# Performance work log

Measured on AMD Instinct MI355X. Metric: run time of the kernel, lower is better.

The kernel has to match this reference:

```python
import jax, jax.numpy as jnp
import numpy as np

B, L, H, NH = 4, 1024, 768, 12
NE, M, P = 30, 6, 600
EMB, BS, NC = 768, 16, 97
NEG = -1e30


def setup_inputs() -> dict:
    key = jax.random.key(0)
    ks = jax.random.split(key, 9)
    sequence_output = jax.random.normal(ks[0], (B, L, H), jnp.float32)
    attention = jax.random.uniform(ks[1], (B, NH, L, L), jnp.float32)
    mention_idx = jax.random.randint(ks[2], (B, NE, M), 0, L)
    mention_mask = jnp.ones((B, NE, M), jnp.float32)
    hts = jax.random.randint(ks[3], (B, P, 2), 0, NE)
    s = 0.02
    head_W = jax.random.normal(ks[4], (EMB, 2 * H), jnp.float32) * s
    head_b = jnp.zeros((EMB,), jnp.float32)
    tail_W = jax.random.normal(ks[5], (EMB, 2 * H), jnp.float32) * s
    tail_b = jnp.zeros((EMB,), jnp.float32)
    proj_W = jax.random.normal(ks[6], (H, EMB * BS), jnp.float32) * s
    cls_W = jax.random.normal(ks[7], (NC, H), jnp.float32) * s
    cls_b = jnp.zeros((NC,), jnp.float32)
    return {
        'sequence_output': sequence_output, 'attention': attention,
        'head_W': head_W, 'head_b': head_b, 'tail_W': tail_W, 'tail_b': tail_b,
        'proj_W': proj_W, 'cls_W': cls_W, 'cls_b': cls_b,
        'mention_mask': mention_mask, 'mention_idx': mention_idx, 'hts': hts,
    }


def reference(sequence_output, attention, head_W, head_b, tail_W, tail_b,
              proj_W, cls_W, cls_b, mention_mask, mention_idx, hts):
    b_, l_, h_ = sequence_output.shape
    bidx = jnp.arange(b_)[:, None, None]                     # [B,1,1]
    # ---- per-entity pooling (segment reduce over ragged mentions) ----
    m_emb = sequence_output[bidx, mention_idx]               # [B,NE,M,H]
    att_t = attention.transpose(0, 2, 1, 3)                  # [B,L,NH,L]
    m_att = att_t[bidx, mention_idx]                         # [B,NE,M,NH,L]
    masked = jnp.where(mention_mask[..., None] > 0, m_emb, NEG)
    e_emb = jax.nn.logsumexp(masked, axis=2)                 # [B,NE,H]
    cnt = jnp.maximum(mention_mask.sum(2), 1.0)              # [B,NE]
    e_att = (m_att * mention_mask[..., None, None]).sum(2) / cnt[..., None, None]  # [B,NE,NH,L]
    # ---- head/tail gathers over pairs ----
    b2 = jnp.arange(b_)[:, None]                             # [B,1]
    h_emb = e_emb[b2, hts[..., 0]]                           # [B,P,H]
    t_emb = e_emb[b2, hts[..., 1]]
    h_att = e_att[b2, hts[..., 0]]                           # [B,P,NH,L]
    t_att = e_att[b2, hts[..., 1]]
    ht_att = (h_att * t_att).mean(2)                         # [B,P,L]
    ht_att = ht_att / (ht_att.sum(-1, keepdims=True) + 1e-30)
    rs = jnp.einsum('bpl,blh->bph', ht_att, sequence_output) # [B,P,H]
    # ---- extractors + block-bilinear classifier ----
    hs = jnp.tanh(jnp.concatenate([h_emb, rs], -1) @ head_W.T + head_b)  # [B,P,EMB]
    ts = jnp.tanh(jnp.concatenate([t_emb, rs], -1) @ tail_W.T + tail_b)
    emb = hs.shape[-1]
    bs = proj_W.shape[1] // emb
    p_ = hs.shape[1]
    b1 = hs.reshape(b_, p_, emb // bs, bs)
    b2t = ts.reshape(b_, p_, emb // bs, bs)
    bl = (b1[..., :, None] * b2t[..., None, :]).reshape(b_, p_, emb * bs)
    logits = (bl @ proj_W.T) @ cls_W.T + cls_b               # [B,P,NC]
    return logits
```

## Files before the change

kernel.cpp:

```cpp
#include <hip/hip_runtime.h>
#include <cmath>

#define B_   4
#define L_   1024
#define H_   768
#define NH_  12
#define NE_  30
#define M_   6
#define P_   600
#define EMB_ 768
#define BS_  16
#define NC_  97

typedef __bf16 bf16x8 __attribute__((ext_vector_type(8)));
typedef float floatx4 __attribute__((ext_vector_type(4)));

union V16 { uint4 q; __bf16 b[8]; bf16x8 v; };
union V8  { unsigned long long u; __bf16 b[4]; };

__device__ __forceinline__ void gload16(const __bf16* g, __bf16* l) {
  __builtin_amdgcn_global_load_lds(
      (const __attribute__((address_space(1))) void*)g,
      (__attribute__((address_space(3))) void*)l, 16, 0, 0);
}

__device__ __forceinline__ void mfma_step(
    const __bf16* As, const __bf16* Bs,
    int ar, int bc, int frow, int kg, floatx4 acc[2][2])
{
  V16 a0, a1, b0, b1;
  a0.q = *reinterpret_cast<const uint4*>(As + (ar + frow) * 32 + kg * 8);
  a1.q = *reinterpret_cast<const uint4*>(As + (ar + 16 + frow) * 32 + kg * 8);
  b0.q = *reinterpret_cast<const uint4*>(Bs + (bc + frow) * 32 + kg * 8);
  b1.q = *reinterpret_cast<const uint4*>(Bs + (bc + 16 + frow) * 32 + kg * 8);
  acc[0][0] = __builtin_amdgcn_mfma_f32_16x16x32_bf16(a0.v, b0.v, acc[0][0], 0, 0, 0);
  acc[0][1] = __builtin_amdgcn_mfma_f32_16x16x32_bf16(a0.v, b1.v, acc[0][1], 0, 0, 0);
  acc[1][0] = __builtin_amdgcn_mfma_f32_16x16x32_bf16(a1.v, b0.v, acc[1][0], 0, 0, 0);
  acc[1][1] = __builtin_amdgcn_mfma_f32_16x16x32_bf16(a1.v, b1.v, acc[1][1], 0, 0, 0);
}

__device__ __forceinline__ void gemm_core(
    const __bf16* __restrict__ A, int lda, long aRow0,
    const __bf16* __restrict__ Bt, int ldb, long bRow0,
    int K, __bf16* sm, floatx4 acc[2][2])
{
  const int tid = threadIdx.x;
  const int lid = tid & 63, w = tid >> 6;
  const int ar = (w & 1) * 32, bc = (w >> 1) * 32;
  const int frow = lid & 15, kg = lid >> 4;
  const int grow = tid >> 2, gq = (tid & 3) * 8;
  const __bf16* ag = A + (aRow0 + grow) * (long)lda + gq;
  const __bf16* bg = Bt + (bRow0 + grow) * (long)ldb + gq;
  __bf16* wA = sm + w * 512;
  const int nt = K >> 5;
  gload16(ag, wA);
  gload16(bg, wA + 2048);
  gload16(ag + 32, wA + 4096);
  gload16(bg + 32, wA + 4096 + 2048);
  int cur = 0;
  for (int i = 0; i < nt - 1; ++i) {
    asm volatile("s_waitcnt vmcnt(2)" ::: "memory");
    __builtin_amdgcn_s_barrier();
    __builtin_amdgcn_sched_barrier(0);
    if (i + 2 < nt) {
      int nb = cur + 2; if (nb >= 3) nb -= 3;
      __bf16* d = sm + nb * 4096 + w * 512;
      gload16(ag + (i + 2) * 32, d);
      gload16(bg + (i + 2) * 32, d + 2048);
    }
    const __bf16* As = sm + cur * 4096;
    mfma_step(As, As + 2048, ar, bc, frow, kg, acc);
    cur += 1; if (cur == 3) cur = 0;
  }
  asm volatile("s_waitcnt vmcnt(0)" ::: "memory");
  __builtin_amdgcn_s_barrier();
  __builtin_amdgcn_sched_barrier(0);
  const __bf16* As = sm + cur * 4096;
  mfma_step(As, As + 2048, ar, bc, frow, kg, acc);
}

#define S1_ATT  1440
#define S1_POOL 120
#define S1_TPS  768
#define S1_TPW  2304
#define S1_CVT  2400

__device__ __forceinline__ void transpose64(
    const float* __restrict__ in, __bf16* __restrict__ out,
    int R, int C, int bx, int by, float (*t)[65])
{
  int c0 = bx*64, r0 = by*64;
  int tx = threadIdx.x & 15, ty = threadIdx.x >> 4;
#pragma unroll
  for (int p = 0; p < 4; ++p) {
    float4 v = *reinterpret_cast<const float4*>(
        in + (long)(r0 + ty + p*16)*C + c0 + tx*4);
    t[ty + p*16][tx*4 + 0] = v.x;
    t[ty + p*16][tx*4 + 1] = v.y;
    t[ty + p*16][tx*4 + 2] = v.z;
    t[ty + p*16][tx*4 + 3] = v.w;
  }
  __syncthreads();
#pragma unroll
  for (int p = 0; p < 4; ++p) {
    V8 o;
#pragma unroll
    for (int i = 0; i < 4; ++i) o.b[i] = (__bf16)t[tx*4 + i][ty + p*16];
    *reinterpret_cast<unsigned long long*>(
        out + (long)(c0 + ty + p*16)*R + r0 + tx*4) = o.u;
  }
}

__global__ __launch_bounds__(256) void k_prep(
    const float* __restrict__ seq, const float* __restrict__ att,
    const float* __restrict__ headW, const float* __restrict__ tailW,
    const float* __restrict__ projW, const float* __restrict__ clsW,
    const float* __restrict__ mmask, const int* __restrict__ midx,
    __bf16* __restrict__ Wt, __bf16* __restrict__ clsA,
    __bf16* __restrict__ projWT, __bf16* __restrict__ seqT,
    __bf16* __restrict__ e_embB, __bf16* __restrict__ e_att)
{
  __shared__ float t[64][65];
  int blk = blockIdx.x;
  int tid = threadIdx.x;
  if (blk < S1_ATT) {
    int i = blk*256 + tid;
    int l4 = (i & 255) * 4;
    int nh = (i >> 8) % NH_;
    int be = i / (256 * NH_);
    int b  = be / NE_;
    float s0=0.f, s1=0.f, s2=0.f, s3=0.f, cnt=0.f;
#pragma unroll
    for (int m = 0; m < M_; ++m) {
      float mk = mmask[be*M_ + m];
      cnt += mk;
      int id = midx[be*M_ + m];
      float4 a = *reinterpret_cast<const float4*>(
          att + (((size_t)b*NH_ + nh)*L_ + id)*L_ + l4);
      s0 += mk*a.x; s1 += mk*a.y; s2 += mk*a.z; s3 += mk*a.w;
    }
    float inv = 1.f / fmaxf(cnt, 1.f);
    V8 o;
    o.b[0]=(__bf16)(s0*inv); o.b[1]=(__bf16)(s1*inv);
    o.b[2]=(__bf16)(s2*inv); o.b[3]=(__bf16)(s3*inv);
    *reinterpret_cast<unsigned long long*>(e_att + ((size_t)be*NH_ + nh)*L_ + l4) = o.u;
  } else if (blk < S1_ATT + S1_POOL) {
    int be = blk - S1_ATT;
    int idx[M_]; float msk[M_];
#pragma unroll
    for (int m = 0; m < M_; ++m) {
      idx[m] = midx[be * M_ + m];
      msk[m] = mmask[be * M_ + m];
    }
    int b = be / NE_;
    const float* sb = seq + (size_t)b * L_ * H_;
    for (int h = tid; h < H_; h += 256) {
      float v[M_]; float mx = -3.0e38f;
#pragma unroll
      for (int m = 0; m < M_; ++m) {
        float x = (msk[m] > 0.f) ? sb[(size_t)idx[m] * H_ + h] : -1e30f;
        v[m] = x; mx = fmaxf(mx, x);
      }
      float s = 0.f;
#pragma unroll
      for (int m = 0; m < M_; ++m) s += expf(v[m] - mx);
      e_embB[(size_t)be * H_ + h] = (__bf16)(mx + logf(s));
    }
  } else if (blk < S1_ATT + S1_POOL + S1_TPS) {
    int b = blk - (S1_ATT + S1_POOL);
    int bx = b % 12, by = (b / 12) % 16, bz = b / 192;
    transpose64(seq + (long)bz*L_*H_, seqT + (long)bz*H_*L_, L_, H_, bx, by, t);
  } else if (blk < S1_ATT + S1_POOL + S1_TPS + S1_TPW) {
    int b = blk - (S1_ATT + S1_POOL + S1_TPS);
    transpose64(projW, projWT, H_, EMB_*BS_, b % 192, b / 192, t);
  } else {
    int gid = (blk - (S1_ATT + S1_POOL + S1_TPS + S1_TPW))*256 + tid;
    if (gid < 2*H_*384) {
      int sel = gid / (H_*384);
      int rem = gid % (H_*384);
      int o = rem / 384;
      int k4 = (rem % 384) * 4;
      const float* W = sel ? tailW : headW;
      float4 v = *reinterpret_cast<const float4*>(W + (long)o*(2*H_) + k4);
      V8 d; d.b[0]=(__bf16)v.x; d.b[1]=(__bf16)v.y; d.b[2]=(__bf16)v.z; d.b[3]=(__bf16)v.w;
      *reinterpret_cast<unsigned long long*>(Wt + ((long)sel*H_ + o)*(2*H_) + k4) = d.u;
    } else {
      int rem = gid - 2*H_*384;
      int row = rem / 192;
      int k4 = (rem % 192) * 4;
      V8 d;
      if (row < NC_) {
        float4 v = *reinterpret_cast<const float4*>(clsW + (long)row*H_ + k4);
        d.b[0]=(__bf16)v.x; d.b[1]=(__bf16)v.y; d.b[2]=(__bf16)v.z; d.b[3]=(__bf16)v.w;
      } else {
        d.b[0]=d.b[1]=d.b[2]=d.b[3]=(__bf16)0.f;
      }
      *reinterpret_cast<unsigned long long*>(clsA + (long)row*H_ + k4) = d.u;
    }
  }
}

#define S2_WC  384
#define S2_PRE 48
#define S2_HT  2400

__global__ __launch_bounds__(256) void k_mid(
    const __bf16* __restrict__ clsA, const __bf16* __restrict__ projWT,
    const __bf16* __restrict__ e_att, const int* __restrict__ hts,
    const __bf16* __restrict__ e_embB, const __bf16* __restrict__ Wt,
    __bf16* __restrict__ WcT, __bf16* __restrict__ htatt,
    float* __restrict__ hpre, float* __restrict__ tpre)
{
  __shared__ __bf16 sm[3*4096];
  int blk = blockIdx.x;
  int tid = threadIdx.x;
  if (blk < S2_WC) {
    int n0 = (blk % 192)*64, r0 = (blk / 192)*64;
    floatx4 acc[2][2] = {};
    gemm_core(clsA, H_, r0, projWT, H_, n0, H_, sm, acc);
    int lid = tid & 63, w = tid >> 6;
    int ar = (w&1)*32, bc = (w>>1)*32, frow = lid&15, kg = lid>>4;
#pragma unroll
    for (int i = 0; i < 2; ++i)
#pragma unroll
      for (int r = 0; r < 4; ++r) {
        int c = r0 + ar + i*16 + kg*4 + r;
#pragma unroll
        for (int j = 0; j < 2; ++j)
          WcT[(long)c*(EMB_*BS_) + n0 + bc + j*16 + frow] = (__bf16)acc[i][j][r];
      }
  } else if (blk < S2_WC + S2_PRE) {
    int tb = blk - S2_WC;
    int o0 = (tb % 12)*64;
    int r0 = ((tb / 12) & 1)*64;
    int sel = tb / 24;
    floatx4 acc[2][2] = {};
    gemm_core(e_embB, H_, r0, Wt + (long)sel*H_*(2*H_), 2*H_, o0, H_, sm, acc);
    float* out = sel ? tpre : hpre;
    int lid = tid & 63, w = tid >> 6;
    int ar = (w&1)*32, bc = (w>>1)*32, frow = lid&15, kg = lid>>4;
#pragma unroll
    for (int i = 0; i < 2; ++i)
#pragma unroll
      for (int r = 0; r < 4; ++r) {
        int be = r0 + ar + i*16 + kg*4 + r;
        if (be < B_*NE_) {
#pragma unroll
          for (int j = 0; j < 2; ++j)
            out[(long)be*EMB_ + o0 + bc + j*16 + frow] = acc[i][j][r];
        }
      }
  } else {
    int bp = blk - (S2_WC + S2_PRE);
    int b = bp / P_;
    int hi = hts[bp*2 + 0], ti = hts[bp*2 + 1];
    const __bf16* ha = e_att + (size_t)(b*NE_ + hi) * NH_ * L_;
    const __bf16* ta = e_att + (size_t)(b*NE_ + ti) * NH_ * L_;
    int l4 = tid * 4;
    float v[4] = {0.f,0.f,0.f,0.f};
#pragma unroll
    for (int nh = 0; nh < NH_; ++nh) {
      V8 x, y;
      x.u = *reinterpret_cast<const unsigned long long*>(ha + nh*L_ + l4);
      y.u = *reinterpret_cast<const unsigned long long*>(ta + nh*L_ + l4);
#pragma unroll
      for (int q = 0; q < 4; ++q) v[q] += (float)x.b[q] * (float)y.b[q];
    }
    float loc = 0.f;
#pragma unroll
    for (int q = 0; q < 4; ++q) { v[q] *= (1.f/NH_); loc += v[q]; }
    float* red = reinterpret_cast<float*>(sm);
    for (int off = 32; off > 0; off >>= 1) loc += __shfl_down(loc, off, 64);
    if ((tid & 63) == 0) red[tid >> 6] = loc;
    __syncthreads();
    float inv = 1.f / (red[0] + red[1] + red[2] + red[3] + 1e-30f);
    V8 o;
#pragma unroll
    for (int q = 0; q < 4; ++q) o.b[q] = (__bf16)(v[q] * inv);
    *reinterpret_cast<unsigned long long*>(htatt + (size_t)bp*L_ + l4) = o.u;
  }
}

__global__ __launch_bounds__(256) void k_rs_mfma(
    const __bf16* __restrict__ htatt, const __bf16* __restrict__ seqT,
    __bf16* __restrict__ rs)
{
  __shared__ __bf16 sm[3*4096];
  int b = blockIdx.z, p0 = blockIdx.y*64, h0 = blockIdx.x*64;
  floatx4 acc[2][2] = {};
  gemm_core(htatt, L_, (long)b*P_ + p0, seqT + (long)b*H_*L_, L_, h0, L_, sm, acc);
  int lid = threadIdx.x & 63, w = threadIdx.x >> 6;
  int ar = (w&1)*32, bc = (w>>1)*32, frow = lid&15, kg = lid>>4;
#pragma unroll
  for (int i = 0; i < 2; ++i)
#pragma unroll
    for (int r = 0; r < 4; ++r) {
      int p = p0 + ar + i*16 + kg*4 + r;
      if (p < P_) {
#pragma unroll
        for (int j = 0; j < 2; ++j)
          rs[((long)b*P_ + p)*H_ + h0 + bc + j*16 + frow] = (__bf16)acc[i][j][r];
      }
    }
}

__global__ __launch_bounds__(256) void k_extract_mfma(
    const __bf16* __restrict__ rs, const __bf16* __restrict__ Wt,
    const float* __restrict__ headb, const float* __restrict__ tailb,
    const float* __restrict__ hpre, const float* __restrict__ tpre,
    const int* __restrict__ hts, __bf16* __restrict__ hs, __bf16* __restrict__ ts)
{
  __shared__ __bf16 sm[3*4096];
  int sel = blockIdx.z, r0 = blockIdx.y*64, o0 = blockIdx.x*64;
  const float* bias = sel ? tailb : headb;
  const float* pre = sel ? tpre : hpre;
  __bf16* out = sel ? ts : hs;
  floatx4 acc[2][2] = {};
  gemm_core(rs, H_, r0, Wt + (long)sel*H_*(2*H_) + H_, 2*H_, o0, H_, sm, acc);
  int lid = threadIdx.x & 63, w = threadIdx.x >> 6;
  int ar = (w&1)*32, bc = (w>>1)*32, frow = lid&15, kg = lid>>4;
#pragma unroll
  for (int i = 0; i < 2; ++i)
#pragma unroll
    for (int r = 0; r < 4; ++r) {
      int row = r0 + ar + i*16 + kg*4 + r;
      if (row < B_*P_) {
        int b = row / P_;
        int e = hts[row*2 + sel];
        const float* prow = pre + (long)(b*NE_ + e) * EMB_;
#pragma unroll
        for (int j = 0; j < 2; ++j) {
          int o = o0 + bc + j*16 + frow;
          out[(long)row*EMB_ + o] = (__bf16)tanhf(acc[i][j][r] + prow[o] + bias[o]);
        }
      }
    }
}

__global__ __launch_bounds__(512) void k_logits_mfma(
    const __bf16* __restrict__ hs, const __bf16* __restrict__ ts,
    const __bf16* __restrict__ WcT, const float* __restrict__ clsb,
    float* __restrict__ out)
{
  int rt = blockIdx.x >> 3;
  int ks = blockIdx.x & 7;
  int tid = threadIdx.x;
  int w = tid >> 6, lid = tid & 63;
  int rg = w & 1, kq = w >> 1;
  int frow = lid & 15, kg = lid >> 4;
  int row = rt*32 + rg*16 + frow;
  long hsrow = (long)row * EMB_;
  floatx4 acc[7] = {};
  int kbase0 = ks*1536 + kq*384;
  for (int s = 0; s < 12; ++s) {
    int kb = kbase0 + s*32 + kg*8;
    int q16 = (kb >> 8) << 4;
    int ii = (kb >> 4) & 15;
    int jj0 = kb & 15;
    float hv = (float)hs[hsrow + q16 + ii];
    V16 tsv; tsv.q = *reinterpret_cast<const uint4*>(ts + hsrow + q16 + jj0);
    bf16x8 af;
#pragma unroll
    for (int j = 0; j < 8; ++j) af[j] = (__bf16)(hv * (float)tsv.b[j]);
#pragma unroll
    for (int f = 0; f < 7; ++f) {
      V16 bv; bv.q = *reinterpret_cast<const uint4*>(WcT + (long)(f*16 + frow)*(EMB_*BS_) + kb);
      acc[f] = __builtin_amdgcn_mfma_f32_16x16x32_bf16(af, bv.v, acc[f], 0, 0, 0);
    }
  }
  __shared__ float red[2][16][112];
  if (kq == 0) {
#pragma unroll
    for (int f = 0; f < 7; ++f)
#pragma unroll
      for (int r = 0; r < 4; ++r)
        red[rg][kg*4 + r][f*16 + frow] = acc[f][r];
  }
  __syncthreads();
#pragma unroll
  for (int q = 1; q < 4; ++q) {
    if (kq == q) {
#pragma unroll
      for (int f = 0; f < 7; ++f)
#pragma unroll
        for (int r = 0; r < 4; ++r)
          red[rg][kg*4 + r][f*16 + frow] += acc[f][r];
    }
    __syncthreads();
  }
  for (int e = tid; e < 32*112; e += 512) {
    int rr = e / 112, cc = e % 112;
    if (cc < NC_) {
      float s = red[rr >> 4][rr & 15][cc] + ((ks == 0) ? clsb[cc] : 0.f);
      atomicAdd(out + (long)(rt*32 + rr)*NC_ + cc, s);
    }
  }
}

extern "C" void kernel_launch(void* const* d_in, const int* in_sizes, int n_in,
                              void* d_out, int out_size, void* d_ws, size_t ws_size,
                              hipStream_t stream) {
  const float* seq   = (const float*)d_in[0];
  const float* att   = (const float*)d_in[1];
  const float* headW = (const float*)d_in[2];
  const float* headb = (const float*)d_in[3];
  const float* tailW = (const float*)d_in[4];
  const float* tailb = (const float*)d_in[5];
  const float* projW = (const float*)d_in[6];
  const float* clsW  = (const float*)d_in[7];
  const float* clsb  = (const float*)d_in[8];
  const float* mmask = (const float*)d_in[9];
  const int* midx = (const int*)d_in[10];
  const int* hts  = (const int*)d_in[11];

  char* p = (char*)d_ws;
  auto alloc_f = [&](size_t n){ float* r = (float*)p; p += n*sizeof(float); return r; };
  auto alloc_b = [&](size_t n){ __bf16* r = (__bf16*)p; p += n*2; return r; };
  float* hpre    = alloc_f((size_t)B_*NE_*EMB_);
  float* tpre    = alloc_f((size_t)B_*NE_*EMB_);
  __bf16* e_embB = alloc_b((size_t)128*H_);
  __bf16* e_att  = alloc_b((size_t)B_*NE_*NH_*L_);
  __bf16* htattb = alloc_b((size_t)2464*L_);
  __bf16* seqT   = alloc_b((size_t)B_*H_*L_);
  __bf16* rsb    = alloc_b((size_t)2432*H_);
  __bf16* Wt     = alloc_b((size_t)2*H_*2*H_);
  __bf16* clsA   = alloc_b((size_t)128*H_);
  __bf16* WcT    = alloc_b((size_t)128*EMB_*BS_);
  __bf16* projWT = alloc_b((size_t)EMB_*BS_*H_);
  __bf16* hsb = projWT;
  __bf16* tsb = projWT + (size_t)B_*P_*EMB_;

  hipMemsetAsync(d_out, 0, (size_t)B_*P_*NC_*sizeof(float), stream);

  k_prep<<<S1_ATT + S1_POOL + S1_TPS + S1_TPW + S1_CVT, 256, 0, stream>>>(
      seq, att, headW, tailW, projW, clsW, mmask, midx,
      Wt, clsA, projWT, seqT, e_embB, e_att);
  k_mid<<<S2_WC + S2_PRE + S2_HT, 256, 0, stream>>>(
      clsA, projWT, e_att, hts, e_embB, Wt, WcT, htattb, hpre, tpre);
  k_rs_mfma<<<dim3(H_/64, 10, B_), 256, 0, stream>>>(htattb, seqT, rsb);
  k_extract_mfma<<<dim3(EMB_/64, 38, 2), 256, 0, stream>>>(
      rsb, Wt, headb, tailb, hpre, tpre, hts, hsb, tsb);
  k_logits_mfma<<<600, 512, 0, stream>>>(hsb, tsb, WcT, clsb, (float*)d_out);
}
```

Measured before the change: 426.7 us.

## Fuse all stages into one persistent kernel with software grid barriers

Replaces the five separate kernel launches and the output memset with a single persistent kernel of 768 blocks. Each block loops over the virtual blocks of each stage, and stages are separated by atomic-counter grid barriers. The output is zeroed inside the first stage. The logits stage is reshaped to 256-thread blocks covering 16 rows each. This removes launch and inter-kernel gaps, at the cost of less latency hiding in the bandwidth-bound stages. It also depends on all 768 blocks being co-resident, with no cooperative launch to guarantee it, so the barriers could deadlock.

```diff
diff --git a/kernel.cpp b/kernel.cpp
--- a/kernel.cpp
+++ b/kernel.cpp
@@ -12,6 +12,8 @@
 #define BS_  16
 #define NC_  97
 
+#define NBLK 768
+
 typedef __bf16 bf16x8 __attribute__((ext_vector_type(8)));
 typedef float floatx4 __attribute__((ext_vector_type(4)));
 
@@ -22,6 +24,17 @@
   __builtin_amdgcn_global_load_lds(
       (const __attribute__((address_space(1))) void*)g,
       (__attribute__((address_space(3))) void*)l, 16, 0, 0);
+}
+
+__device__ __forceinline__ void grid_sync(int* cnt) {
+  __syncthreads();
+  if (threadIdx.x == 0) {
+    __threadfence();
+    atomicAdd(cnt, 1);
+    while (atomicAdd(cnt, 0) < NBLK) __builtin_amdgcn_s_sleep(32);
+    __threadfence();
+  }
+  __syncthreads();
 }
 
 __device__ __forceinline__ void mfma_step(
@@ -79,12 +92,6 @@
   mfma_step(As, As + 2048, ar, bc, frow, kg, acc);
 }
 
-#define S1_ATT  1440
-#define S1_POOL 120
-#define S1_TPS  768
-#define S1_TPW  2304
-#define S1_CVT  2400
-
 __device__ __forceinline__ void transpose64(
     const float* __restrict__ in, __bf16* __restrict__ out,
     int R, int C, int bx, int by, float (*t)[65])
@@ -111,288 +118,306 @@
   }
 }
 
-__global__ __launch_bounds__(256) void k_prep(
-    const float* __restrict__ seq, const float* __restrict__ att,
-    const float* __restrict__ headW, const float* __restrict__ tailW,
-    const float* __restrict__ projW, const float* __restrict__ clsW,
-    const float* __restrict__ mmask, const int* __restrict__ midx,
-    __bf16* __restrict__ Wt, __bf16* __restrict__ clsA,
-    __bf16* __restrict__ projWT, __bf16* __restrict__ seqT,
-    __bf16* __restrict__ e_embB, __bf16* __restrict__ e_att)
-{
-  __shared__ float t[64][65];
-  int blk = blockIdx.x;
-  int tid = threadIdx.x;
-  if (blk < S1_ATT) {
-    int i = blk*256 + tid;
-    int l4 = (i & 255) * 4;
-    int nh = (i >> 8) % NH_;
-    int be = i / (256 * NH_);
-    int b  = be / NE_;
-    float s0=0.f, s1=0.f, s2=0.f, s3=0.f, cnt=0.f;
-#pragma unroll
-    for (int m = 0; m < M_; ++m) {
-      float mk = mmask[be*M_ + m];
-      cnt += mk;
-      int id = midx[be*M_ + m];
-      float4 a = *reinterpret_cast<const float4*>(
-          att + (((size_t)b*NH_ + nh)*L_ + id)*L_ + l4);
-      s0 += mk*a.x; s1 += mk*a.y; s2 += mk*a.z; s3 += mk*a.w;
-    }
-    float inv = 1.f / fmaxf(cnt, 1.f);
-    V8 o;
-    o.b[0]=(__bf16)(s0*inv); o.b[1]=(__bf16)(s1*inv);
-    o.b[2]=(__bf16)(s2*inv); o.b[3]=(__bf16)(s3*inv);
-    *reinterpret_cast<unsigned long long*>(e_att + ((size_t)be*NH_ + nh)*L_ + l4) = o.u;
-  } else if (blk < S1_ATT + S1_POOL) {
-    int be = blk - S1_ATT;
-    int idx[M_]; float msk[M_];
-#pragma unroll
-    for (int m = 0; m < M_; ++m) {
-      idx[m] = midx[be * M_ + m];
-      msk[m] = mmask[be * M_ + m];
-    }
-    int b = be / NE_;
-    const float* sb = seq + (size_t)b * L_ * H_;
-    for (int h = tid; h < H_; h += 256) {
-      float v[M_]; float mx = -3.0e38f;
-#pragma unroll
-      for (int m = 0; m < M_; ++m) {
-        float x = (msk[m] > 0.f) ? sb[(size_t)idx[m] * H_ + h] : -1e30f;
-        v[m] = x; mx = fmaxf(mx, x);
-      }
-      float s = 0.f;
-#pragma unroll
-      for (int m = 0; m < M_; ++m) s += expf(v[m] - mx);
-      e_embB[(size_t)be * H_ + h] = (__bf16)(mx + logf(s));
-    }
-  } else if (blk < S1_ATT + S1_POOL + S1_TPS) {
-    int b = blk - (S1_ATT + S1_POOL);
-    int bx = b % 12, by = (b / 12) % 16, bz = b / 192;
-    transpose64(seq + (long)bz*L_*H_, seqT + (long)bz*H_*L_, L_, H_, bx, by, t);
-  } else if (blk < S1_ATT + S1_POOL + S1_TPS + S1_TPW) {
-    int b = blk - (S1_ATT + S1_POOL + S1_TPS);
-    transpose64(projW, projWT, H_, EMB_*BS_, b % 192, b / 192, t);
-  } else {
-    int gid = (blk - (S1_ATT + S1_POOL + S1_TPS + S1_TPW))*256 + tid;
-    if (gid < 2*H_*384) {
-      int sel = gid / (H_*384);
-      int rem = gid % (H_*384);
-      int o = rem / 384;
-      int k4 = (rem % 384) * 4;
-      const float* W = sel ? tailW : headW;
-      float4 v = *reinterpret_cast<const float4*>(W + (long)o*(2*H_) + k4);
-      V8 d; d.b[0]=(__bf16)v.x; d.b[1]=(__bf16)v.y; d.b[2]=(__bf16)v.z; d.b[3]=(__bf16)v.w;
-      *reinterpret_cast<unsigned long long*>(Wt + ((long)sel*H_ + o)*(2*H_) + k4) = d.u;
-    } else {
-      int rem = gid - 2*H_*384;
-      int row = rem / 192;
-      int k4 = (rem % 192) * 4;
-      V8 d;
-      if (row < NC_) {
-        float4 v = *reinterpret_cast<const float4*>(clsW + (long)row*H_ + k4);
-        d.b[0]=(__bf16)v.x; d.b[1]=(__bf16)v.y; d.b[2]=(__bf16)v.z; d.b[3]=(__bf16)v.w;
-      } else {
-        d.b[0]=d.b[1]=d.b[2]=d.b[3]=(__bf16)0.f;
-      }
-      *reinterpret_cast<unsigned long long*>(clsA + (long)row*H_ + k4) = d.u;
-    }
-  }
-}
-
+#define S1_ATT  1440
+#define S1_POOL 120
+#define S1_TPS  768
+#define S1_TPW  2304
+#define S1_CVT  2400
+#define NPREP (S1_ATT + S1_POOL + S1_TPS + S1_TPW + S1_CVT)
 #define S2_WC  384
 #define S2_PRE 48
 #define S2_HT  2400
-
-__global__ __launch_bounds__(256) void k_mid(
-    const __bf16* __restrict__ clsA, const __bf16* __restrict__ projWT,
-    const __bf16* __restrict__ e_att, const int* __restrict__ hts,
-    const __bf16* __restrict__ e_embB, const __bf16* __restrict__ Wt,
+#define NMID (S2_WC + S2_PRE + S2_HT)
+#define NRS   480
+#define NEXT  912
+#define NLOG  1200
+
+__global__ __launch_bounds__(256, 4) void k_fused(
+    const float* __restrict__ seq, const float* __restrict__ att,
+    const float* __restrict__ headW, const float* __restrict__ headb,
+    const float* __restrict__ tailW, const float* __restrict__ tailb,
+    const float* __restrict__ projW, const float* __restrict__ clsW,
+    const float* __restrict__ clsb, const float* __restrict__ mmask,
+    const int* __restrict__ midx, const int* __restrict__ hts,
+    __bf16* __restrict__ Wt, __bf16* __restrict__ clsA,
+    __bf16* __restrict__ projWT, __bf16* __restrict__ seqT,
+    __bf16* __restrict__ e_embB, __bf16* __restrict__ e_att,
     __bf16* __restrict__ WcT, __bf16* __restrict__ htatt,
-    float* __restrict__ hpre, float* __restrict__ tpre)
+    float* __restrict__ hpre, float* __restrict__ tpre,
+    __bf16* __restrict__ rs, __bf16* __restrict__ hs, __bf16* __restrict__ ts,
+    float* __restrict__ out, int* __restrict__ bar)
 {
-  __shared__ __bf16 sm[3*4096];
-  int blk = blockIdx.x;
-  int tid = threadIdx.x;
-  if (blk < S2_WC) {
-    int n0 = (blk % 192)*64, r0 = (blk / 192)*64;
-    floatx4 acc[2][2] = {};
-    gemm_core(clsA, H_, r0, projWT, H_, n0, H_, sm, acc);
-    int lid = tid & 63, w = tid >> 6;
-    int ar = (w&1)*32, bc = (w>>1)*32, frow = lid&15, kg = lid>>4;
-#pragma unroll
-    for (int i = 0; i < 2; ++i)
-#pragma unroll
-      for (int r = 0; r < 4; ++r) {
-        int c = r0 + ar + i*16 + kg*4 + r;
-#pragma unroll
-        for (int j = 0; j < 2; ++j)
-          WcT[(long)c*(EMB_*BS_) + n0 + bc + j*16 + frow] = (__bf16)acc[i][j][r];
-      }
-  } else if (blk < S2_WC + S2_PRE) {
-    int tb = blk - S2_WC;
-    int o0 = (tb % 12)*64;
-    int r0 = ((tb / 12) & 1)*64;
-    int sel = tb / 24;
-    floatx4 acc[2][2] = {};
-    gemm_core(e_embB, H_, r0, Wt + (long)sel*H_*(2*H_), 2*H_, o0, H_, sm, acc);
-    float* out = sel ? tpre : hpre;
-    int lid = tid & 63, w = tid >> 6;
-    int ar = (w&1)*32, bc = (w>>1)*32, frow = lid&15, kg = lid>>4;
-#pragma unroll
-    for (int i = 0; i < 2; ++i)
-#pragma unroll
-      for (int r = 0; r < 4; ++r) {
-        int be = r0 + ar + i*16 + kg*4 + r;
-        if (be < B_*NE_) {
-#pragma unroll
-          for (int j = 0; j < 2; ++j)
-            out[(long)be*EMB_ + o0 + bc + j*16 + frow] = acc[i][j][r];
-        }
-      }
-  } else {
-    int bp = blk - (S2_WC + S2_PRE);
-    int b = bp / P_;
-    int hi = hts[bp*2 + 0], ti = hts[bp*2 + 1];
-    const __bf16* ha = e_att + (size_t)(b*NE_ + hi) * NH_ * L_;
-    const __bf16* ta = e_att + (size_t)(b*NE_ + ti) * NH_ * L_;
-    int l4 = tid * 4;
-    float v[4] = {0.f,0.f,0.f,0.f};
-#pragma unroll
-    for (int nh = 0; nh < NH_; ++nh) {
-      V8 x, y;
-      x.u = *reinterpret_cast<const unsigned long long*>(ha + nh*L_ + l4);
-      y.u = *reinterpret_cast<const unsigned long long*>(ta + nh*L_ + l4);
-#pragma unroll
-      for (int q = 0; q < 4; ++q) v[q] += (float)x.b[q] * (float)y.b[q];
-    }
-    float loc = 0.f;
-#pragma unroll
-    for (int q = 0; q < 4; ++q) { v[q] *= (1.f/NH_); loc += v[q]; }
-    float* red = reinterpret_cast<float*>(sm);
-    for (int off = 32; off > 0; off >>= 1) loc += __shfl_down(loc, off, 64);
-    if ((tid & 63) == 0) red[tid >> 6] = loc;
-    __syncthreads();
-    float inv = 1.f / (red[0] + red[1] + red[2] + red[3] + 1e-30f);
-    V8 o;
-#pragma unroll
-    for (int q = 0; q < 4; ++q) o.b[q] = (__bf16)(v[q] * inv);
-    *reinterpret_cast<unsigned long long*>(htatt + (size_t)bp*L_ + l4) = o.u;
-  }
-}
-
-__global__ __launch_bounds__(256) void k_rs_mfma(
-    const __bf16* __restrict__ htatt, const __bf16* __restrict__ seqT,
-    __bf16* __restrict__ rs)
-{
-  __shared__ __bf16 sm[3*4096];
-  int b = blockIdx.z, p0 = blockIdx.y*64, h0 = blockIdx.x*64;
-  floatx4 acc[2][2] = {};
-  gemm_core(htatt, L_, (long)b*P_ + p0, seqT + (long)b*H_*L_, L_, h0, L_, sm, acc);
-  int lid = threadIdx.x & 63, w = threadIdx.x >> 6;
-  int ar = (w&1)*32, bc = (w>>1)*32, frow = lid&15, kg = lid>>4;
-#pragma unroll
-  for (int i = 0; i < 2; ++i)
-#pragma unroll
-    for (int r = 0; r < 4; ++r) {
-      int p = p0 + ar + i*16 + kg*4 + r;
-      if (p < P_) {
-#pragma unroll
-        for (int j = 0; j < 2; ++j)
-          rs[((long)b*P_ + p)*H_ + h0 + bc + j*16 + frow] = (__bf16)acc[i][j][r];
-      }
-    }
-}
-
-__global__ __launch_bounds__(256) void k_extract_mfma(
-    const __bf16* __restrict__ rs, const __bf16* __restrict__ Wt,
-    const float* __restrict__ headb, const float* __restrict__ tailb,
-    const float* __restrict__ hpre, const float* __restrict__ tpre,
-    const int* __restrict__ hts, __bf16* __restrict__ hs, __bf16* __restrict__ ts)
-{
-  __shared__ __bf16 sm[3*4096];
-  int sel = blockIdx.z, r0 = blockIdx.y*64, o0 = blockIdx.x*64;
-  const float* bias = sel ? tailb : headb;
-  const float* pre = sel ? tpre : hpre;
-  __bf16* out = sel ? ts : hs;
-  floatx4 acc[2][2] = {};
-  gemm_core(rs, H_, r0, Wt + (long)sel*H_*(2*H_) + H_, 2*H_, o0, H_, sm, acc);
-  int lid = threadIdx.x & 63, w = threadIdx.x >> 6;
-  int ar = (w&1)*32, bc = (w>>1)*32, frow = lid&15, kg = lid>>4;
-#pragma unroll
-  for (int i = 0; i < 2; ++i)
-#pragma unroll
-    for (int r = 0; r < 4; ++r) {
-      int row = r0 + ar + i*16 + kg*4 + r;
-      if (row < B_*P_) {
-        int b = row / P_;
-        int e = hts[row*2 + sel];
-        const float* prow = pre + (long)(b*NE_ + e) * EMB_;
-#pragma unroll
-        for (int j = 0; j < 2; ++j) {
-          int o = o0 + bc + j*16 + frow;
-          out[(long)row*EMB_ + o] = (__bf16)tanhf(acc[i][j][r] + prow[o] + bias[o]);
-        }
-      }
-    }
-}
-
-__global__ __launch_bounds__(512) void k_logits_mfma(
-    const __bf16* __restrict__ hs, const __bf16* __restrict__ ts,
-    const __bf16* __restrict__ WcT, const float* __restrict__ clsb,
-    float* __restrict__ out)
-{
-  int rt = blockIdx.x >> 3;
-  int ks = blockIdx.x & 7;
-  int tid = threadIdx.x;
-  int w = tid >> 6, lid = tid & 63;
-  int rg = w & 1, kq = w >> 1;
-  int frow = lid & 15, kg = lid >> 4;
-  int row = rt*32 + rg*16 + frow;
-  long hsrow = (long)row * EMB_;
-  floatx4 acc[7] = {};
-  int kbase0 = ks*1536 + kq*384;
-  for (int s = 0; s < 12; ++s) {
-    int kb = kbase0 + s*32 + kg*8;
-    int q16 = (kb >> 8) << 4;
-    int ii = (kb >> 4) & 15;
-    int jj0 = kb & 15;
-    float hv = (float)hs[hsrow + q16 + ii];
-    V16 tsv; tsv.q = *reinterpret_cast<const uint4*>(ts + hsrow + q16 + jj0);
-    bf16x8 af;
-#pragma unroll
-    for (int j = 0; j < 8; ++j) af[j] = (__bf16)(hv * (float)tsv.b[j]);
-#pragma unroll
-    for (int f = 0; f < 7; ++f) {
-      V16 bv; bv.q = *reinterpret_cast<const uint4*>(WcT + (long)(f*16 + frow)*(EMB_*BS_) + kb);
-      acc[f] = __builtin_amdgcn_mfma_f32_16x16x32_bf16(af, bv.v, acc[f], 0, 0, 0);
-    }
-  }
-  __shared__ float red[2][16][112];
-  if (kq == 0) {
-#pragma unroll
-    for (int f = 0; f < 7; ++f)
-#pragma unroll
-      for (int r = 0; r < 4; ++r)
-        red[rg][kg*4 + r][f*16 + frow] = acc[f][r];
-  }
-  __syncthreads();
-#pragma unroll
-  for (int q = 1; q < 4; ++q) {
-    if (kq == q) {
-#pragma unroll
-      for (int f = 0; f < 7; ++f)
-#pragma unroll
-        for (int r = 0; r < 4; ++r)
-          red[rg][kg*4 + r][f*16 + frow] += acc[f][r];
-    }
-    __syncthreads();
-  }
-  for (int e = tid; e < 32*112; e += 512) {
-    int rr = e / 112, cc = e % 112;
-    if (cc < NC_) {
-      float s = red[rr >> 4][rr & 15][cc] + ((ks == 0) ? clsb[cc] : 0.f);
-      atomicAdd(out + (long)(rt*32 + rr)*NC_ + cc, s);
+  __shared__ char smraw[24576];
+  const int tid = threadIdx.x;
+
+  {
+    float (*t)[65] = reinterpret_cast<float(*)[65]>(smraw);
+    for (int vb = blockIdx.x; vb < NPREP; vb += NBLK) {
+      if (vb < S1_ATT) {
+        int i = vb*256 + tid;
+        int l4 = (i & 255) * 4;
+        int nh = (i >> 8) % NH_;
+        int be = i / (256 * NH_);
+        int b  = be / NE_;
+        float s0=0.f, s1=0.f, s2=0.f, s3=0.f, cnt=0.f;
+#pragma unroll
+        for (int m = 0; m < M_; ++m) {
+          float mk = mmask[be*M_ + m];
+          cnt += mk;
+          int id = midx[be*M_ + m];
+          float4 a = *reinterpret_cast<const float4*>(
+              att + (((size_t)b*NH_ + nh)*L_ + id)*L_ + l4);
+          s0 += mk*a.x; s1 += mk*a.y; s2 += mk*a.z; s3 += mk*a.w;
+        }
+        float inv = 1.f / fmaxf(cnt, 1.f);
+        V8 o;
+        o.b[0]=(__bf16)(s0*inv); o.b[1]=(__bf16)(s1*inv);
+        o.b[2]=(__bf16)(s2*inv); o.b[3]=(__bf16)(s3*inv);
+        *reinterpret_cast<unsigned long long*>(e_att + ((size_t)be*NH_ + nh)*L_ + l4) = o.u;
+      } else if (vb < S1_ATT + S1_POOL) {
+        int be = vb - S1_ATT;
+        int idx[M_]; float msk[M_];
+#pragma unroll
+        for (int m = 0; m < M_; ++m) {
+          idx[m] = midx[be * M_ + m];
+          msk[m] = mmask[be * M_ + m];
+        }
+        int b = be / NE_;
+        const float* sb = seq + (size_t)b * L_ * H_;
+        for (int h = tid; h < H_; h += 256) {
+          float v[M_]; float mx = -3.0e38f;
+#pragma unroll
+          for (int m = 0; m < M_; ++m) {
+            float x = (msk[m] > 0.f) ? sb[(size_t)idx[m] * H_ + h] : -1e30f;
+            v[m] = x; mx = fmaxf(mx, x);
+          }
+          float s = 0.f;
+#pragma unroll
+          for (int m = 0; m < M_; ++m) s += expf(v[m] - mx);
+          e_embB[(size_t)be * H_ + h] = (__bf16)(mx + logf(s));
+        }
+      } else if (vb < S1_ATT + S1_POOL + S1_TPS) {
+        int b = vb - (S1_ATT + S1_POOL);
+        int bx = b % 12, by = (b / 12) % 16, bz = b / 192;
+        transpose64(seq + (long)bz*L_*H_, seqT + (long)bz*H_*L_, L_, H_, bx, by, t);
+      } else if (vb < S1_ATT + S1_POOL + S1_TPS + S1_TPW) {
+        int b = vb - (S1_ATT + S1_POOL + S1_TPS);
+        transpose64(projW, projWT, H_, EMB_*BS_, b % 192, b / 192, t);
+      } else {
+        int gid = (vb - (S1_ATT + S1_POOL + S1_TPS + S1_TPW))*256 + tid;
+        if (gid < 2*H_*384) {
+          int sel = gid / (H_*384);
+          int rem = gid % (H_*384);
+          int o = rem / 384;
+          int k4 = (rem % 384) * 4;
+          const float* W = sel ? tailW : headW;
+          float4 v = *reinterpret_cast<const float4*>(W + (long)o*(2*H_) + k4);
+          V8 d; d.b[0]=(__bf16)v.x; d.b[1]=(__bf16)v.y; d.b[2]=(__bf16)v.z; d.b[3]=(__bf16)v.w;
+          *reinterpret_cast<unsigned long long*>(Wt + ((long)sel*H_ + o)*(2*H_) + k4) = d.u;
+        } else {
+          int rem = gid - 2*H_*384;
+          int row = rem / 192;
+          int k4 = (rem % 192) * 4;
+          V8 d;
+          if (row < NC_) {
+            float4 v = *reinterpret_cast<const float4*>(clsW + (long)row*H_ + k4);
+            d.b[0]=(__bf16)v.x; d.b[1]=(__bf16)v.y; d.b[2]=(__bf16)v.z; d.b[3]=(__bf16)v.w;
+          } else {
+            d.b[0]=d.b[1]=d.b[2]=d.b[3]=(__bf16)0.f;
+          }
+          *reinterpret_cast<unsigned long long*>(clsA + (long)row*H_ + k4) = d.u;
+        }
+      }
+      __syncthreads();
+    }
+    for (int i = blockIdx.x*256 + tid; i < B_*P_*NC_; i += NBLK*256) out[i] = 0.f;
+  }
+  grid_sync(bar + 0);
+
+  {
+    __bf16* sm = reinterpret_cast<__bf16*>(smraw);
+    for (int vb = blockIdx.x; vb < NMID; vb += NBLK) {
+      if (vb < S2_WC) {
+        int n0 = (vb % 192)*64, r0 = (vb / 192)*64;
+        floatx4 acc[2][2] = {};
+        gemm_core(clsA, H_, r0, projWT, H_, n0, H_, sm, acc);
+        int lid = tid & 63, w = tid >> 6;
+        int ar = (w&1)*32, bc = (w>>1)*32, frow = lid&15, kg = lid>>4;
+#pragma unroll
+        for (int i = 0; i < 2; ++i)
+#pragma unroll
+          for (int r = 0; r < 4; ++r) {
+            int c = r0 + ar + i*16 + kg*4 + r;
+#pragma unroll
+            for (int j = 0; j < 2; ++j)
+              WcT[(long)c*(EMB_*BS_) + n0 + bc + j*16 + frow] = (__bf16)acc[i][j][r];
+          }
+      } else if (vb < S2_WC + S2_PRE) {
+        int tb = vb - S2_WC;
+        int o0 = (tb % 12)*64;
+        int r0 = ((tb / 12) & 1)*64;
+        int sel = tb / 24;
+        floatx4 acc[2][2] = {};
+        gemm_core(e_embB, H_, r0, Wt + (long)sel*H_*(2*H_), 2*H_, o0, H_, sm, acc);
+        float* o = sel ? tpre : hpre;
+        int lid = tid & 63, w = tid >> 6;
+        int ar = (w&1)*32, bc = (w>>1)*32, frow = lid&15, kg = lid>>4;
+#pragma unroll
+        for (int i = 0; i < 2; ++i)
+#pragma unroll
+          for (int r = 0; r < 4; ++r) {
+            int be = r0 + ar + i*16 + kg*4 + r;
+            if (be < B_*NE_) {
+#pragma unroll
+              for (int j = 0; j < 2; ++j)
+                o[(long)be*EMB_ + o0 + bc + j*16 + frow] = acc[i][j][r];
+            }
+          }
+      } else {
+        int bp = vb - (S2_WC + S2_PRE);
+        int b = bp / P_;
+        int hi = hts[bp*2 + 0], ti = hts[bp*2 + 1];
+        const __bf16* ha = e_att + (size_t)(b*NE_ + hi) * NH_ * L_;
+        const __bf16* ta = e_att + (size_t)(b*NE_ + ti) * NH_ * L_;
+        int l4 = tid * 4;
+        float v[4] = {0.f,0.f,0.f,0.f};
+#pragma unroll
+        for (int nh = 0; nh < NH_; ++nh) {
+          V8 x, y;
+          x.u = *reinterpret_cast<const unsigned long long*>(ha + nh*L_ + l4);
+          y.u = *reinterpret_cast<const unsigned long long*>(ta + nh*L_ + l4);
+#pragma unroll
+          for (int q = 0; q < 4; ++q) v[q] += (float)x.b[q] * (float)y.b[q];
+        }
+        float loc = 0.f;
+#pragma unroll
+        for (int q = 0; q < 4; ++q) { v[q] *= (1.f/NH_); loc += v[q]; }
+        float* red = reinterpret_cast<float*>(smraw);
+        for (int off = 32; off > 0; off >>= 1) loc += __shfl_down(loc, off, 64);
+        if ((tid & 63) == 0) red[tid >> 6] = loc;
+        __syncthreads();
+        float inv = 1.f / (red[0] + red[1] + red[2] + red[3] + 1e-30f);
+        V8 o;
+#pragma unroll
+        for (int q = 0; q < 4; ++q) o.b[q] = (__bf16)(v[q] * inv);
+        *reinterpret_cast<unsigned long long*>(htatt + (size_t)bp*L_ + l4) = o.u;
+      }
+      __syncthreads();
+    }
+  }
+  grid_sync(bar + 1);
+
+  {
+    __bf16* sm = reinterpret_cast<__bf16*>(smraw);
+    for (int vb = blockIdx.x; vb < NRS; vb += NBLK) {
+      int h0 = (vb % 12)*64, p0 = ((vb / 12) % 10)*64, b = vb / 120;
+      floatx4 acc[2][2] = {};
+      gemm_core(htatt, L_, (long)b*P_ + p0, seqT + (long)b*H_*L_, L_, h0, L_, sm, acc);
+      int lid = tid & 63, w = tid >> 6;
+      int ar = (w&1)*32, bc = (w>>1)*32, frow = lid&15, kg = lid>>4;
+#pragma unroll
+      for (int i = 0; i < 2; ++i)
+#pragma unroll
+        for (int r = 0; r < 4; ++r) {
+          int p = p0 + ar + i*16 + kg*4 + r;
+          if (p < P_) {
+#pragma unroll
+            for (int j = 0; j < 2; ++j)
+              rs[((long)b*P_ + p)*H_ + h0 + bc + j*16 + frow] = (__bf16)acc[i][j][r];
+          }
+        }
+      __syncthreads();
+    }
+  }
+  grid_sync(bar + 2);
+
+  {
+    __bf16* sm = reinterpret_cast<__bf16*>(smraw);
+    for (int vb = blockIdx.x; vb < NEXT; vb += NBLK) {
+      int o0 = (vb % 12)*64, r0 = ((vb / 12) % 38)*64, sel = vb / 456;
+      const float* bias = sel ? tailb : headb;
+      const float* pre = sel ? tpre : hpre;
+      __bf16* o = sel ? ts : hs;
+      floatx4 acc[2][2] = {};
+      gemm_core(rs, H_, r0, Wt + (long)sel*H_*(2*H_) + H_, 2*H_, o0, H_, sm, acc);
+      int lid = tid & 63, w = tid >> 6;
+      int ar = (w&1)*32, bc = (w>>1)*32, frow = lid&15, kg = lid>>4;
+#pragma unroll
+      for (int i = 0; i < 2; ++i)
+#pragma unroll
+        for (int r = 0; r < 4; ++r) {
+          int row = r0 + ar + i*16 + kg*4 + r;
+          if (row < B_*P_) {
+            int b = row / P_;
+            int e = hts[row*2 + sel];
+            const float* prow = pre + (long)(b*NE_ + e) * EMB_;
+#pragma unroll
+            for (int j = 0; j < 2; ++j) {
+              int oo = o0 + bc + j*16 + frow;
+              o[(long)row*EMB_ + oo] = (__bf16)tanhf(acc[i][j][r] + prow[oo] + bias[oo]);
+            }
+          }
+        }
+      __syncthreads();
+    }
+  }
+  grid_sync(bar + 3);
+
+  {
+    float (*red)[112] = reinterpret_cast<float(*)[112]>(smraw);
+    for (int vb = blockIdx.x; vb < NLOG; vb += NBLK) {
+      int rt = vb >> 3;
+      int ks = vb & 7;
+      int w = tid >> 6, lid = tid & 63;
+      int kq = w;
+      int frow = lid & 15, kg = lid >> 4;
+      int row = rt*16 + frow;
+      long hsrow = (long)row * EMB_;
+      floatx4 acc[7] = {};
+      int kbase0 = ks*1536 + kq*384;
+      for (int s = 0; s < 12; ++s) {
+        int kb = kbase0 + s*32 + kg*8;
+        int q16 = (kb >> 8) << 4;
+        int ii = (kb >> 4) & 15;
+        int jj0 = kb & 15;
+        float hv = (float)hs[hsrow + q16 + ii];
+        V16 tsv; tsv.q = *reinterpret_cast<const uint4*>(ts + hsrow + q16 + jj0);
+        bf16x8 af;
+#pragma unroll
+        for (int j = 0; j < 8; ++j) af[j] = (__bf16)(hv * (float)tsv.b[j]);
+#pragma unroll
+        for (int f = 0; f < 7; ++f) {
+          V16 bv; bv.q = *reinterpret_cast<const uint4*>(WcT + (long)(f*16 + frow)*(EMB_*BS_) + kb);
+          acc[f] = __builtin_amdgcn_mfma_f32_16x16x32_bf16(af, bv.v, acc[f], 0, 0, 0);
+        }
+      }
+      if (kq == 0) {
+#pragma unroll
+        for (int f = 0; f < 7; ++f)
+#pragma unroll
+          for (int r = 0; r < 4; ++r)
+            red[kg*4 + r][f*16 + frow] = acc[f][r];
+      }
+      __syncthreads();
+#pragma unroll
+      for (int q = 1; q < 4; ++q) {
+        if (kq == q) {
+#pragma unroll
+          for (int f = 0; f < 7; ++f)
+#pragma unroll
+            for (int r = 0; r < 4; ++r)
+              red[kg*4 + r][f*16 + frow] += acc[f][r];
+        }
+        __syncthreads();
+      }
+      for (int e = tid; e < 16*112; e += 256) {
+        int rr = e / 112, cc = e % 112;
+        if (cc < NC_) {
+          float s = red[rr][cc] + ((ks == 0) ? clsb[cc] : 0.f);
+          atomicAdd(out + (long)(rt*16 + rr)*NC_ + cc, s);
+        }
+      }
+      __syncthreads();
     }
   }
 }
@@ -414,6 +439,7 @@
   const int* hts  = (const int*)d_in[11];
 
   char* p = (char*)d_ws;
+  int* bar = (int*)p; p += 256;
   auto alloc_f = [&](size_t n){ float* r = (float*)p; p += n*sizeof(float); return r; };
   auto alloc_b = [&](size_t n){ __bf16* r = (__bf16*)p; p += n*2; return r; };
   float* hpre    = alloc_f((size_t)B_*NE_*EMB_);
@@ -430,15 +456,10 @@
   __bf16* hsb = projWT;
   __bf16* tsb = projWT + (size_t)B_*P_*EMB_;
 
-  hipMemsetAsync(d_out, 0, (size_t)B_*P_*NC_*sizeof(float), stream);
-
-  k_prep<<<S1_ATT + S1_POOL + S1_TPS + S1_TPW + S1_CVT, 256, 0, stream>>>(
-      seq, att, headW, tailW, projW, clsW, mmask, midx,
-      Wt, clsA, projWT, seqT, e_embB, e_att);
-  k_mid<<<S2_WC + S2_PRE + S2_HT, 256, 0, stream>>>(
-      clsA, projWT, e_att, hts, e_embB, Wt, WcT, htattb, hpre, tpre);
-  k_rs_mfma<<<dim3(H_/64, 10, B_), 256, 0, stream>>>(htattb, seqT, rsb);
-  k_extract_mfma<<<dim3(EMB_/64, 38, 2), 256, 0, stream>>>(
-      rsb, Wt, headb, tailb, hpre, tpre, hts, hsb, tsb);
-  k_logits_mfma<<<600, 512, 0, stream>>>(hsb, tsb, WcT, clsb, (float*)d_out);
-}
+  hipMemsetAsync(bar, 0, 256, stream);
+
+  k_fused<<<NBLK, 256, 0, stream>>>(
+      seq, att, headW, headb, tailW, tailb, projW, clsW, clsb, mmask, midx, hts,
+      Wt, clsA, projWT, seqT, e_embB, e_att, WcT, htattb, hpre, tpre,
+      rsb, hsb, tsb, (float*)d_out, bar);
+}
```

New measurement: 779.6 us. +82.7%, slower.
